# Kernel tuning notes

Hardware: AMD Instinct MI355X
Metric: run time of the kernel (lower is better)

## Reference

```python
import jax, jax.numpy as jnp
import numpy as np

EMB_DIM = 768
NUM_HEADS = 12
OUT_DIM = 768


def setup_inputs() -> dict:
    key = jax.random.key(0)
    k_x, k_q, k_k, k_v, k_o = jax.random.split(key, 5)
    B, N, D = 8, 1024, EMB_DIM
    s = 1.0 / np.sqrt(D)
    return {
        "x": jax.random.normal(k_x, (B, N, D), dtype=jnp.float32),
        # torch nn.Linear weights are stored [out_features, in_features]
        "Wq": jax.random.normal(k_q, (D, D), dtype=jnp.float32) * s,
        "Wk": jax.random.normal(k_k, (D, D), dtype=jnp.float32) * s,
        "Wv": jax.random.normal(k_v, (D, D), dtype=jnp.float32) * s,
        "Wo": jax.random.normal(k_o, (OUT_DIM, D), dtype=jnp.float32) * s,
    }


def _split_heads(t, H):
    # [B, N, D] -> [B*H, N, D//H]  (heads folded into batch, per einsum 'b i d')
    B, N, D = t.shape
    return t.reshape(B, N, H, D // H).transpose(0, 2, 1, 3).reshape(B * H, N, D // H)


def _merge_heads(t, B, H):
    BH, N, dh = t.shape
    return t.reshape(B, H, N, dh).transpose(0, 2, 1, 3).reshape(B, N, H * dh)


def reference(x, Wq, Wk, Wv, Wo):
    B, N, D = x.shape
    H = NUM_HEADS
    dh = D // H
    # q/k/v projections (torch Linear: y = x @ W.T, no bias)
    q = _split_heads(x @ Wq.T, H)
    k = _split_heads(x @ Wk.T, H)
    v = _split_heads(x @ Wv.T, H)
    scale = dh ** (-0.5)
    # dots: 'b i d , b j d -> b i j' -> full [B*H, N, N] score matrix
    dots = jnp.einsum('bid,bjd->bij', q, k) * scale
    attn = jax.nn.softmax(dots, axis=-1)
    # dropout p=0.0 -> identity
    # vect: 'b i d , b d j -> b i j' == attn @ v
    vect = jnp.einsum('bij,bjd->bid', attn, v)
    out = _merge_heads(vect, B, H) @ Wo.T
    return out
```

## Files before the change

kernel.cpp:

```cpp
#include <hip/hip_runtime.h>
#include <hip/hip_bf16.h>
#include <stdint.h>


typedef __bf16 bf16x8 __attribute__((ext_vector_type(8)));
typedef __bf16 bf16x4 __attribute__((ext_vector_type(4)));
typedef float f32x4 __attribute__((ext_vector_type(4)));

#define GAS __attribute__((address_space(1)))
#define LAS __attribute__((address_space(3)))

__device__ __forceinline__ void glds16(const short* gp, short* lp) {
  __builtin_amdgcn_global_load_lds((const GAS void*)gp, (LAS void*)lp, 16, 0, 0);
}

__device__ __forceinline__ float fast_exp2(float x) {
#if __has_builtin(__builtin_amdgcn_exp2f)
  return __builtin_amdgcn_exp2f(x);
#else
  return __expf(x * 0.6931471805599453f);
#endif
}

__device__ __forceinline__ short bfbits(float f) {
  __bf16 b = (__bf16)f;
  union { __bf16 b; short s; } cv; cv.b = b;
  return cv.s;
}

__device__ __forceinline__ void stage8_f32(const float* __restrict__ src, short* dst) {
  float4 f0 = ((const float4*)src)[0];
  float4 f1 = ((const float4*)src)[1];
  bf16x8 t;
  t[0] = (__bf16)f0.x; t[1] = (__bf16)f0.y; t[2] = (__bf16)f0.z; t[3] = (__bf16)f0.w;
  t[4] = (__bf16)f1.x; t[5] = (__bf16)f1.y; t[6] = (__bf16)f1.z; t[7] = (__bf16)f1.w;
  *(bf16x8*)dst = t;
}

__global__ __launch_bounds__(256) void convert_kernel(
    const float* __restrict__ x, const float* __restrict__ Wq,
    const float* __restrict__ Wk, const float* __restrict__ Wv,
    const float* __restrict__ Wo,
    short* __restrict__ xb, short* __restrict__ wqkv, short* __restrict__ wob) {
  int seg = blockIdx.y;
  const float* src; short* dst; int n8;
  if (seg == 0) { src = x; dst = xb; n8 = 786432; }
  else if (seg == 4) { src = Wo; dst = wob; n8 = 73728; }
  else {
    src = (seg == 1) ? Wq : (seg == 2) ? Wk : Wv;
    dst = wqkv + (size_t)(seg - 1) * 589824;
    n8 = 73728;
  }
  int idx = blockIdx.x * 256 + threadIdx.x;
  if (idx >= n8) return;
  stage8_f32(src + (size_t)idx * 8, dst + (size_t)idx * 8);
}

__global__ __launch_bounds__(256) void gemm_qkv(
    const short* __restrict__ xb, const short* __restrict__ wqkv,
    short* __restrict__ q, short* __restrict__ k, short* __restrict__ vt) {
  const int m0 = blockIdx.x * 128;
  const int by = blockIdx.y;
  const int n0g = by * 128;
  const int tid = threadIdx.x;
  const int w = tid >> 6, lane = tid & 63, l16 = lane & 15, quad = lane >> 4;
  const int wr = w >> 1, wc = w & 1;

  __shared__ short sA[128 * 64];
  __shared__ short sB[128 * 64];

  f32x4 acc[4][4];
#pragma unroll
  for (int i = 0; i < 4; ++i)
#pragma unroll
    for (int j = 0; j < 4; ++j) acc[i][j] = (f32x4){0.f, 0.f, 0.f, 0.f};

  for (int k0 = 0; k0 < 768; k0 += 64) {
    __syncthreads();
    const short* Ab = xb + (size_t)m0 * 768 + k0;
    const short* Bb = wqkv + (size_t)n0g * 768 + k0;
#pragma unroll
    for (int p = 0; p < 4; ++p) {
      int lin = (w * 4 + p) * 64 + lane;
      int row = lin >> 3;
      int cs = ((lin & 7) ^ (row & 7)) * 8;
      glds16(Ab + (size_t)row * 768 + cs, &sA[lin * 8]);
      glds16(Bb + (size_t)row * 768 + cs, &sB[lin * 8]);
    }
    __syncthreads();
#pragma unroll
    for (int kk2 = 0; kk2 < 2; ++kk2) {
      bf16x8 af[4], bfg[4];
#pragma unroll
      for (int t = 0; t < 4; ++t) {
        int ra = wr * 64 + t * 16 + l16;
        af[t] = *(const bf16x8*)&sA[ra * 64 + (((kk2 * 4 + quad) ^ (ra & 7)) << 3)];
        int rb = wc * 64 + t * 16 + l16;
        bfg[t] = *(const bf16x8*)&sB[rb * 64 + (((kk2 * 4 + quad) ^ (rb & 7)) << 3)];
      }
#pragma unroll
      for (int ti = 0; ti < 4; ++ti)
#pragma unroll
        for (int tj = 0; tj < 4; ++tj)
          acc[ti][tj] = __builtin_amdgcn_mfma_f32_16x16x32_bf16(af[ti], bfg[tj], acc[ti][tj], 0, 0, 0);
    }
  }

  const int wsel = by / 6;
  const int nl0 = (by % 6) * 128 + wc * 64;
  if (wsel == 2) {
#pragma unroll
    for (int ti = 0; ti < 4; ++ti)
#pragma unroll
      for (int tj = 0; tj < 4; ++tj) {
        int token = m0 + wr * 64 + ti * 16 + quad * 4;
        int nl = nl0 + tj * 16 + l16;
        int bh = (token >> 10) * 12 + (nl >> 6);
        short tmp[4];
#pragma unroll
        for (int r = 0; r < 4; ++r) tmp[r] = bfbits(acc[ti][tj][r]);
        *(uint2*)(vt + (size_t)bh * 65536 + (size_t)(nl & 63) * 1024 + (token & 1023)) =
            *(const uint2*)tmp;
      }
  } else {
    short* C = wsel ? k : q;
    const float sc = wsel ? 1.0f : 0.1803368801111244f;
#pragma unroll
    for (int ti = 0; ti < 4; ++ti)
#pragma unroll
      for (int tj = 0; tj < 4; ++tj)
#pragma unroll
        for (int r = 0; r < 4; ++r) {
          int row = m0 + wr * 64 + ti * 16 + quad * 4 + r;
          int nl = nl0 + tj * 16 + l16;
          C[(size_t)row * 768 + nl] = bfbits(acc[ti][tj][r] * sc);
        }
  }
}

__global__ __launch_bounds__(256) void attn_kernel(
    const short* __restrict__ q, const short* __restrict__ k,
    const short* __restrict__ vt, short* __restrict__ vect) {
  const int bh = blockIdx.x % 96;
  const int qt = blockIdx.x / 96;
  const int b = bh / 12, h = bh % 12;
  const int m0 = qt * 128;
  const int tid = threadIdx.x;
  const int w = tid >> 6, lane = tid & 63, l16 = lane & 15, quad = lane >> 4;

  __shared__ short sQ[128 * 64];
  __shared__ short sK[2][64 * 64];
  __shared__ short sVt[2][64 * 64];

  const size_t base = (size_t)b * 786432 + (size_t)h * 64;
  const size_t vbase = (size_t)bh * 65536;

#pragma unroll
  for (int p = 0; p < 4; ++p) {
    int lin = (w * 4 + p) * 64 + lane;
    int row = lin >> 3;
    int cs = ((lin & 7) ^ (row & 7)) * 8;
    glds16(q + base + (size_t)(m0 + row) * 768 + cs, &sQ[lin * 8]);
  }
#pragma unroll
  for (int p = 0; p < 2; ++p) {
    int lin = (w * 2 + p) * 64 + lane;
    int row = lin >> 3;
    int cs = ((lin & 7) ^ (row & 7)) * 8;
    glds16(k + base + (size_t)row * 768 + cs, &sK[0][lin * 8]);
    glds16(vt + vbase + (size_t)row * 1024 + cs, &sVt[0][lin * 8]);
  }
  __syncthreads();

  bf16x8 bq[2][2];
#pragma unroll
  for (int g = 0; g < 2; ++g)
#pragma unroll
    for (int kk = 0; kk < 2; ++kk) {
      int row = w * 32 + g * 16 + l16;
      bq[g][kk] = *(const bf16x8*)&sQ[row * 64 + (((kk * 4 + quad) ^ (row & 7)) << 3)];
    }

  f32x4 l4[2];
  f32x4 oacc[2][4];
#pragma unroll
  for (int g = 0; g < 2; ++g) {
    l4[g] = (f32x4){0.f, 0.f, 0.f, 0.f};
#pragma unroll
    for (int td = 0; td < 4; ++td) oacc[g][td] = (f32x4){0.f, 0.f, 0.f, 0.f};
  }

  for (int t = 0; t < 16; ++t) {
    if (t < 15) {
      int j0n = (t + 1) * 64;
      short* sKn = sK[(t + 1) & 1];
      short* sVn = sVt[(t + 1) & 1];
#pragma unroll
      for (int p = 0; p < 2; ++p) {
        int lin = (w * 2 + p) * 64 + lane;
        int row = lin >> 3;
        int cs = ((lin & 7) ^ (row & 7)) * 8;
        glds16(k + base + (size_t)(j0n + row) * 768 + cs, &sKn[lin * 8]);
        glds16(vt + vbase + (size_t)row * 1024 + j0n + cs, &sVn[lin * 8]);
      }
    }
    const short* sKc = sK[t & 1];
    const short* sVc = sVt[t & 1];

    f32x4 s[2][4];
#pragma unroll
    for (int g = 0; g < 2; ++g)
#pragma unroll
      for (int ti = 0; ti < 4; ++ti) s[g][ti] = (f32x4){0.f, 0.f, 0.f, 0.f};
#pragma unroll
    for (int kk = 0; kk < 2; ++kk)
#pragma unroll
      for (int ti = 0; ti < 4; ++ti) {
        int row = ti * 16 + l16;
        bf16x8 a = *(const bf16x8*)&sKc[row * 64 + (((kk * 4 + quad) ^ (row & 7)) << 3)];
        s[0][ti] = __builtin_amdgcn_mfma_f32_16x16x32_bf16(a, bq[0][kk], s[0][ti], 0, 0, 0);
        s[1][ti] = __builtin_amdgcn_mfma_f32_16x16x32_bf16(a, bq[1][kk], s[1][ti], 0, 0, 0);
      }

    bf16x4 pb[2][4];
#pragma unroll
    for (int g = 0; g < 2; ++g)
#pragma unroll
      for (int ti = 0; ti < 4; ++ti) {
        f32x4 e;
        e[0] = fast_exp2(s[g][ti][0]);
        e[1] = fast_exp2(s[g][ti][1]);
        e[2] = fast_exp2(s[g][ti][2]);
        e[3] = fast_exp2(s[g][ti][3]);
        l4[g] += e;
        bf16x4 tb;
        tb[0] = (__bf16)e[0]; tb[1] = (__bf16)e[1];
        tb[2] = (__bf16)e[2]; tb[3] = (__bf16)e[3];
        pb[g][ti] = tb;
      }

#pragma unroll
    for (int t2 = 0; t2 < 2; ++t2) {
      bf16x8 av[4];
#pragma unroll
      for (int td = 0; td < 4; ++td) {
        int row = td * 16 + l16;
        int o1 = t2 * 32 + quad * 4;
        int c1 = o1 >> 3, w1 = o1 & 7;
        int c2 = c1 + 2;
        union { uint2 u[2]; bf16x8 v; } tmp;
        tmp.u[0] = *(const uint2*)&sVc[row * 64 + ((c1 ^ (row & 7)) << 3) + w1];
        tmp.u[1] = *(const uint2*)&sVc[row * 64 + ((c2 ^ (row & 7)) << 3) + w1];
        av[td] = tmp.v;
      }
#pragma unroll
      for (int g = 0; g < 2; ++g) {
        union { bf16x4 h[2]; bf16x8 v; } bp;
        bp.h[0] = pb[g][2 * t2];
        bp.h[1] = pb[g][2 * t2 + 1];
#pragma unroll
        for (int td = 0; td < 4; ++td)
          oacc[g][td] = __builtin_amdgcn_mfma_f32_16x16x32_bf16(av[td], bp.v, oacc[g][td], 0, 0, 0);
      }
    }
    if (t < 15) __syncthreads();
  }

#pragma unroll
  for (int g = 0; g < 2; ++g) {
    float l = (l4[g][0] + l4[g][1]) + (l4[g][2] + l4[g][3]);
    l += __shfl_xor(l, 16);
    l += __shfl_xor(l, 32);
    float inv = 1.0f / l;
    int i_tok = m0 + w * 32 + g * 16 + l16;
#pragma unroll
    for (int td = 0; td < 4; ++td) {
      short tmp[4];
#pragma unroll
      for (int r = 0; r < 4; ++r) tmp[r] = bfbits(oacc[g][td][r] * inv);
      *(uint2*)(vect + base + (size_t)i_tok * 768 + td * 16 + quad * 4) = *(const uint2*)tmp;
    }
  }
}

__global__ __launch_bounds__(256) void gemm_out(
    const short* __restrict__ vect, const short* __restrict__ wob,
    float* __restrict__ out) {
  const int m0 = blockIdx.x * 64;
  const int n0 = blockIdx.y * 128;
  const int tid = threadIdx.x;
  const int w = tid >> 6, lane = tid & 63, l16 = lane & 15, quad = lane >> 4;
  const int wr = w >> 1, wc = w & 1;

  __shared__ short sA[64 * 64];
  __shared__ short sB[128 * 64];

  f32x4 acc[2][4];
#pragma unroll
  for (int i = 0; i < 2; ++i)
#pragma unroll
    for (int j = 0; j < 4; ++j) acc[i][j] = (f32x4){0.f, 0.f, 0.f, 0.f};

  for (int k0 = 0; k0 < 768; k0 += 64) {
    __syncthreads();
    const short* Ab = vect + (size_t)m0 * 768 + k0;
    const short* Bb = wob + (size_t)n0 * 768 + k0;
#pragma unroll
    for (int p = 0; p < 2; ++p) {
      int lin = (w * 2 + p) * 64 + lane;
      int row = lin >> 3;
      int cs = ((lin & 7) ^ (row & 7)) * 8;
      glds16(Ab + (size_t)row * 768 + cs, &sA[lin * 8]);
    }
#pragma unroll
    for (int p = 0; p < 4; ++p) {
      int lin = (w * 4 + p) * 64 + lane;
      int row = lin >> 3;
      int cs = ((lin & 7) ^ (row & 7)) * 8;
      glds16(Bb + (size_t)row * 768 + cs, &sB[lin * 8]);
    }
    __syncthreads();
#pragma unroll
    for (int kk2 = 0; kk2 < 2; ++kk2) {
      bf16x8 af[2], bfg[4];
#pragma unroll
      for (int t = 0; t < 2; ++t) {
        int ra = wr * 32 + t * 16 + l16;
        af[t] = *(const bf16x8*)&sA[ra * 64 + (((kk2 * 4 + quad) ^ (ra & 7)) << 3)];
      }
#pragma unroll
      for (int t = 0; t < 4; ++t) {
        int rb = wc * 64 + t * 16 + l16;
        bfg[t] = *(const bf16x8*)&sB[rb * 64 + (((kk2 * 4 + quad) ^ (rb & 7)) << 3)];
      }
#pragma unroll
      for (int ti = 0; ti < 2; ++ti)
#pragma unroll
        for (int tj = 0; tj < 4; ++tj)
          acc[ti][tj] = __builtin_amdgcn_mfma_f32_16x16x32_bf16(af[ti], bfg[tj], acc[ti][tj], 0, 0, 0);
    }
  }
#pragma unroll
  for (int ti = 0; ti < 2; ++ti)
#pragma unroll
    for (int tj = 0; tj < 4; ++tj)
#pragma unroll
      for (int r = 0; r < 4; ++r) {
        int row = m0 + wr * 32 + ti * 16 + quad * 4 + r;
        int col = n0 + wc * 64 + tj * 16 + l16;
        out[(size_t)row * 768 + col] = acc[ti][tj][r];
      }
}

extern "C" void kernel_launch(void* const* d_in, const int* in_sizes, int n_in,
                              void* d_out, int out_size, void* d_ws, size_t ws_size,
                              hipStream_t stream) {
  const float* x  = (const float*)d_in[0];
  const float* Wq = (const float*)d_in[1];
  const float* Wk = (const float*)d_in[2];
  const float* Wv = (const float*)d_in[3];
  const float* Wo = (const float*)d_in[4];
  float* out = (float*)d_out;

  const size_t MN = (size_t)8192 * 768;
  short* q    = (short*)d_ws;
  short* k    = q + MN;
  short* vt   = k + MN;
  short* vect = q;
  short* wob  = vt + MN;

  short* xb   = (short*)d_out;
  short* wqkv = xb + MN;

  convert_kernel<<<dim3(3072, 5), 256, 0, stream>>>(x, Wq, Wk, Wv, Wo, xb, wqkv, wob);
  gemm_qkv<<<dim3(64, 18), 256, 0, stream>>>(xb, wqkv, q, k, vt);
  attn_kernel<<<768, 256, 0, stream>>>(q, k, vt, vect);
  gemm_out<<<dim3(128, 6), 256, 0, stream>>>(vect, wob, out);
}
```

Before: 201.1 us.

## Halve attention query tile, drop K/V double buffering, flatten convert kernel

The attention kernel now processes 64 query rows per block instead of 128, with one 16-row group per wave, and launches twice as many blocks. K/V tiles are single-buffered and loaded synchronously with two barriers per step instead of prefetched into a double buffer. The convert kernel is rewritten as a flat grid in which each thread converts four 8-element chunks, so no blocks are wasted on the short weight segments. The smaller tile lowers register and LDS use, which may raise occupancy, but it doubles K/V traffic per query and gives up the load/compute overlap.

After: 196.9 us. -2.0%, faster.

```diff
diff --git a/kernel.cpp b/kernel.cpp
--- a/kernel.cpp
+++ b/kernel.cpp
@@ -42,18 +42,24 @@
     const float* __restrict__ Wk, const float* __restrict__ Wv,
     const float* __restrict__ Wo,
     short* __restrict__ xb, short* __restrict__ wqkv, short* __restrict__ wob) {
-  int seg = blockIdx.y;
-  const float* src; short* dst; int n8;
-  if (seg == 0) { src = x; dst = xb; n8 = 786432; }
-  else if (seg == 4) { src = Wo; dst = wob; n8 = 73728; }
-  else {
-    src = (seg == 1) ? Wq : (seg == 2) ? Wk : Wv;
-    dst = wqkv + (size_t)(seg - 1) * 589824;
-    n8 = 73728;
-  }
-  int idx = blockIdx.x * 256 + threadIdx.x;
-  if (idx >= n8) return;
-  stage8_f32(src + (size_t)idx * 8, dst + (size_t)idx * 8);
+  int u0 = blockIdx.x * 1024 + threadIdx.x;
+#pragma unroll
+  for (int i = 0; i < 4; ++i) {
+    int u = u0 + i * 256;
+    const float* src; short* dst;
+    if (u < 786432) { src = x + (size_t)u * 8; dst = xb + (size_t)u * 8; }
+    else if (u < 1007616) {
+      int r = u - 786432;
+      int wsel = r / 73728, off = r % 73728;
+      const float* W = (wsel == 0) ? Wq : (wsel == 1) ? Wk : Wv;
+      src = W + (size_t)off * 8;
+      dst = wqkv + (size_t)r * 8;
+    } else {
+      int r = u - 1007616;
+      src = Wo + (size_t)r * 8; dst = wob + (size_t)r * 8;
+    }
+    stage8_f32(src, dst);
+  }
 }
 
 __global__ __launch_bounds__(256) void gemm_qkv(
@@ -144,104 +150,81 @@
   const int bh = blockIdx.x % 96;
   const int qt = blockIdx.x / 96;
   const int b = bh / 12, h = bh % 12;
-  const int m0 = qt * 128;
+  const int m0 = qt * 64;
   const int tid = threadIdx.x;
   const int w = tid >> 6, lane = tid & 63, l16 = lane & 15, quad = lane >> 4;
 
-  __shared__ short sQ[128 * 64];
-  __shared__ short sK[2][64 * 64];
-  __shared__ short sVt[2][64 * 64];
+  __shared__ short sQ[64 * 64];
+  __shared__ short sK[64 * 64];
+  __shared__ short sVt[64 * 64];
 
   const size_t base = (size_t)b * 786432 + (size_t)h * 64;
   const size_t vbase = (size_t)bh * 65536;
 
-#pragma unroll
-  for (int p = 0; p < 4; ++p) {
-    int lin = (w * 4 + p) * 64 + lane;
-    int row = lin >> 3;
-    int cs = ((lin & 7) ^ (row & 7)) * 8;
-    glds16(q + base + (size_t)(m0 + row) * 768 + cs, &sQ[lin * 8]);
-  }
 #pragma unroll
   for (int p = 0; p < 2; ++p) {
     int lin = (w * 2 + p) * 64 + lane;
     int row = lin >> 3;
     int cs = ((lin & 7) ^ (row & 7)) * 8;
-    glds16(k + base + (size_t)row * 768 + cs, &sK[0][lin * 8]);
-    glds16(vt + vbase + (size_t)row * 1024 + cs, &sVt[0][lin * 8]);
+    glds16(q + base + (size_t)(m0 + row) * 768 + cs, &sQ[lin * 8]);
   }
   __syncthreads();
-
-  bf16x8 bq[2][2];
-#pragma unroll
-  for (int g = 0; g < 2; ++g)
-#pragma unroll
-    for (int kk = 0; kk < 2; ++kk) {
-      int row = w * 32 + g * 16 + l16;
-      bq[g][kk] = *(const bf16x8*)&sQ[row * 64 + (((kk * 4 + quad) ^ (row & 7)) << 3)];
-    }
-
-  f32x4 l4[2];
-  f32x4 oacc[2][4];
-#pragma unroll
-  for (int g = 0; g < 2; ++g) {
-    l4[g] = (f32x4){0.f, 0.f, 0.f, 0.f};
-#pragma unroll
-    for (int td = 0; td < 4; ++td) oacc[g][td] = (f32x4){0.f, 0.f, 0.f, 0.f};
-  }
-
-  for (int t = 0; t < 16; ++t) {
-    if (t < 15) {
-      int j0n = (t + 1) * 64;
-      short* sKn = sK[(t + 1) & 1];
-      short* sVn = sVt[(t + 1) & 1];
-#pragma unroll
-      for (int p = 0; p < 2; ++p) {
-        int lin = (w * 2 + p) * 64 + lane;
-        int row = lin >> 3;
-        int cs = ((lin & 7) ^ (row & 7)) * 8;
-        glds16(k + base + (size_t)(j0n + row) * 768 + cs, &sKn[lin * 8]);
-        glds16(vt + vbase + (size_t)row * 1024 + j0n + cs, &sVn[lin * 8]);
-      }
-    }
-    const short* sKc = sK[t & 1];
-    const short* sVc = sVt[t & 1];
-
-    f32x4 s[2][4];
-#pragma unroll
-    for (int g = 0; g < 2; ++g)
-#pragma unroll
-      for (int ti = 0; ti < 4; ++ti) s[g][ti] = (f32x4){0.f, 0.f, 0.f, 0.f};
+  bf16x8 bq[2];
+#pragma unroll
+  for (int kk = 0; kk < 2; ++kk) {
+    int row = w * 16 + l16;
+    bq[kk] = *(const bf16x8*)&sQ[row * 64 + (((kk * 4 + quad) ^ (row & 7)) << 3)];
+  }
+
+  f32x4 l4 = (f32x4){0.f, 0.f, 0.f, 0.f};
+  f32x4 oacc[4];
+#pragma unroll
+  for (int td = 0; td < 4; ++td) oacc[td] = (f32x4){0.f, 0.f, 0.f, 0.f};
+
+  for (int j0 = 0; j0 < 1024; j0 += 64) {
+    __syncthreads();
+#pragma unroll
+    for (int p = 0; p < 2; ++p) {
+      int lin = (w * 2 + p) * 64 + lane;
+      int row = lin >> 3;
+      int cs = ((lin & 7) ^ (row & 7)) * 8;
+      glds16(k + base + (size_t)(j0 + row) * 768 + cs, &sK[lin * 8]);
+      glds16(vt + vbase + (size_t)row * 1024 + j0 + cs, &sVt[lin * 8]);
+    }
+    __syncthreads();
+
+    f32x4 s[4];
+#pragma unroll
+    for (int ti = 0; ti < 4; ++ti) s[ti] = (f32x4){0.f, 0.f, 0.f, 0.f};
 #pragma unroll
     for (int kk = 0; kk < 2; ++kk)
 #pragma unroll
       for (int ti = 0; ti < 4; ++ti) {
         int row = ti * 16 + l16;
-        bf16x8 a = *(const bf16x8*)&sKc[row * 64 + (((kk * 4 + quad) ^ (row & 7)) << 3)];
-        s[0][ti] = __builtin_amdgcn_mfma_f32_16x16x32_bf16(a, bq[0][kk], s[0][ti], 0, 0, 0);
-        s[1][ti] = __builtin_amdgcn_mfma_f32_16x16x32_bf16(a, bq[1][kk], s[1][ti], 0, 0, 0);
-      }
-
-    bf16x4 pb[2][4];
-#pragma unroll
-    for (int g = 0; g < 2; ++g)
-#pragma unroll
-      for (int ti = 0; ti < 4; ++ti) {
-        f32x4 e;
-        e[0] = fast_exp2(s[g][ti][0]);
-        e[1] = fast_exp2(s[g][ti][1]);
-        e[2] = fast_exp2(s[g][ti][2]);
-        e[3] = fast_exp2(s[g][ti][3]);
-        l4[g] += e;
-        bf16x4 tb;
-        tb[0] = (__bf16)e[0]; tb[1] = (__bf16)e[1];
-        tb[2] = (__bf16)e[2]; tb[3] = (__bf16)e[3];
-        pb[g][ti] = tb;
-      }
+        bf16x8 a = *(const bf16x8*)&sK[row * 64 + (((kk * 4 + quad) ^ (row & 7)) << 3)];
+        s[ti] = __builtin_amdgcn_mfma_f32_16x16x32_bf16(a, bq[kk], s[ti], 0, 0, 0);
+      }
+
+    bf16x4 pb[4];
+#pragma unroll
+    for (int ti = 0; ti < 4; ++ti) {
+      f32x4 e;
+      e[0] = fast_exp2(s[ti][0]);
+      e[1] = fast_exp2(s[ti][1]);
+      e[2] = fast_exp2(s[ti][2]);
+      e[3] = fast_exp2(s[ti][3]);
+      l4 += e;
+      bf16x4 tb;
+      tb[0] = (__bf16)e[0]; tb[1] = (__bf16)e[1];
+      tb[2] = (__bf16)e[2]; tb[3] = (__bf16)e[3];
+      pb[ti] = tb;
+    }
 
 #pragma unroll
     for (int t2 = 0; t2 < 2; ++t2) {
-      bf16x8 av[4];
+      union { bf16x4 h[2]; bf16x8 v; } bp;
+      bp.h[0] = pb[2 * t2];
+      bp.h[1] = pb[2 * t2 + 1];
 #pragma unroll
       for (int td = 0; td < 4; ++td) {
         int row = td * 16 + l16;
@@ -249,37 +232,24 @@
         int c1 = o1 >> 3, w1 = o1 & 7;
         int c2 = c1 + 2;
         union { uint2 u[2]; bf16x8 v; } tmp;
-        tmp.u[0] = *(const uint2*)&sVc[row * 64 + ((c1 ^ (row & 7)) << 3) + w1];
-        tmp.u[1] = *(const uint2*)&sVc[row * 64 + ((c2 ^ (row & 7)) << 3) + w1];
-        av[td] = tmp.v;
-      }
-#pragma unroll
-      for (int g = 0; g < 2; ++g) {
-        union { bf16x4 h[2]; bf16x8 v; } bp;
-        bp.h[0] = pb[g][2 * t2];
-        bp.h[1] = pb[g][2 * t2 + 1];
-#pragma unroll
-        for (int td = 0; td < 4; ++td)
-          oacc[g][td] = __builtin_amdgcn_mfma_f32_16x16x32_bf16(av[td], bp.v, oacc[g][td], 0, 0, 0);
-      }
-    }
-    if (t < 15) __syncthreads();
-  }
-
-#pragma unroll
-  for (int g = 0; g < 2; ++g) {
-    float l = (l4[g][0] + l4[g][1]) + (l4[g][2] + l4[g][3]);
-    l += __shfl_xor(l, 16);
-    l += __shfl_xor(l, 32);
-    float inv = 1.0f / l;
-    int i_tok = m0 + w * 32 + g * 16 + l16;
-#pragma unroll
-    for (int td = 0; td < 4; ++td) {
-      short tmp[4];
-#pragma unroll
-      for (int r = 0; r < 4; ++r) tmp[r] = bfbits(oacc[g][td][r] * inv);
-      *(uint2*)(vect + base + (size_t)i_tok * 768 + td * 16 + quad * 4) = *(const uint2*)tmp;
-    }
+        tmp.u[0] = *(const uint2*)&sVt[row * 64 + ((c1 ^ (row & 7)) << 3) + w1];
+        tmp.u[1] = *(const uint2*)&sVt[row * 64 + ((c2 ^ (row & 7)) << 3) + w1];
+        oacc[td] = __builtin_amdgcn_mfma_f32_16x16x32_bf16(tmp.v, bp.v, oacc[td], 0, 0, 0);
+      }
+    }
+  }
+
+  float l = (l4[0] + l4[1]) + (l4[2] + l4[3]);
+  l += __shfl_xor(l, 16);
+  l += __shfl_xor(l, 32);
+  float inv = 1.0f / l;
+  int i_tok = m0 + w * 16 + l16;
+#pragma unroll
+  for (int td = 0; td < 4; ++td) {
+    short tmp[4];
+#pragma unroll
+    for (int r = 0; r < 4; ++r) tmp[r] = bfbits(oacc[td][r] * inv);
+    *(uint2*)(vect + base + (size_t)i_tok * 768 + td * 16 + quad * 4) = *(const uint2*)tmp;
   }
 }
 
@@ -372,8 +342,8 @@
   short* xb   = (short*)d_out;
   short* wqkv = xb + MN;
 
-  convert_kernel<<<dim3(3072, 5), 256, 0, stream>>>(x, Wq, Wk, Wv, Wo, xb, wqkv, wob);
+  convert_kernel<<<1056, 256, 0, stream>>>(x, Wq, Wk, Wv, Wo, xb, wqkv, wob);
   gemm_qkv<<<dim3(64, 18), 256, 0, stream>>>(xb, wqkv, q, k, vt);
-  attn_kernel<<<768, 256, 0, stream>>>(q, k, vt, vect);
+  attn_kernel<<<1536, 256, 0, stream>>>(q, k, vt, vect);
   gemm_out<<<dim3(128, 6), 256, 0, stream>>>(vect, wob, out);
 }
```
